# Performance work log

Hardware: AMD Instinct MI355X
Metric: run time of the kernel (lower is better)

Reference implementation:

```python
import jax, jax.numpy as jnp
import numpy as np

BATCH = 2
L = 2048
D_MODEL = 1024
D_STATE = 16
D_CONV = 4
EXPAND = 2
D_INNER = EXPAND * D_MODEL  # 2048
DT_RANK = (D_MODEL + 15) // 16  # 64


def setup_inputs() -> dict:
    key = jax.random.key(0)
    ks = jax.random.split(key, 12)
    f = jnp.float32
    hidden_states = jax.random.normal(ks[0], (BATCH, L, D_MODEL), f)
    input2 = jax.random.normal(ks[1], (BATCH, L, D_MODEL), f)
    in_proj1_w = jax.random.normal(ks[2], (D_INNER, D_MODEL), f) * (D_MODEL ** -0.5)
    in_proj2_w = jax.random.normal(ks[3], (D_INNER, D_MODEL), f) * (D_MODEL ** -0.5)
    conv_w = jax.random.normal(ks[4], (D_INNER, 1, D_CONV), f) * (D_CONV ** -0.5)
    conv_b = jax.random.normal(ks[5], (D_INNER,), f) * 0.02
    x_proj_w = jax.random.normal(ks[6], (DT_RANK + 2 * D_STATE, D_INNER), f) * (D_INNER ** -0.5)
    dt_std = DT_RANK ** -0.5
    dt_proj_w = jax.random.uniform(ks[7], (D_INNER, DT_RANK), f, -dt_std, dt_std)
    # dt bias init: inverse softplus of log-uniform dt in [1e-3, 1e-1]
    dt = jnp.exp(jax.random.uniform(ks[8], (D_INNER,), f) * (np.log(0.1) - np.log(0.001)) + np.log(0.001))
    dt = jnp.clip(dt, 1e-4, None)
    dt_proj_b = dt + jnp.log(-jnp.expm1(-dt))
    # A_log init: log(1..d_state) broadcast over channels
    A_log = jnp.log(jnp.broadcast_to(jnp.arange(1, D_STATE + 1, dtype=f), (D_INNER, D_STATE)))
    D = jnp.ones((D_INNER,), f)
    out_proj_w = jax.random.normal(ks[9], (D_MODEL, D_INNER), f) * (D_INNER ** -0.5)
    return dict(hidden_states=hidden_states, input2=input2, in_proj1_w=in_proj1_w,
                in_proj2_w=in_proj2_w, conv_w=conv_w, conv_b=conv_b, x_proj_w=x_proj_w,
                dt_proj_w=dt_proj_w, dt_proj_b=dt_proj_b, A_log=A_log, D=D,
                out_proj_w=out_proj_w)


def _forward(hidden_states, input2, in_proj1_w, in_proj2_w, conv_w, conv_b,
             x_proj_w, dt_proj_w, dt_proj_b, A_log, D, out_proj_w):
    # in_proj: (B,L,Dm) -> (B,d_inner,L)
    x = jnp.einsum('bld,ed->bel', hidden_states, in_proj1_w)
    z = jnp.einsum('bld,ed->bel', input2, in_proj2_w)
    # causal depthwise conv1d (left pad d_conv-1, equiv to torch pad+truncate) + SiLU
    xc = jax.lax.conv_general_dilated(x, conv_w, (1,), [(D_CONV - 1, 0)],
                                      dimension_numbers=('NCH', 'OIH', 'NCH'),
                                      feature_group_count=D_INNER)
    x = jax.nn.silu(xc + conv_b[None, :, None])
    # x_proj -> dt, B, C
    x_dbl = jnp.einsum('bel,re->brl', x, x_proj_w)  # (B, dt_rank+2n, L)
    dt = x_dbl[:, :DT_RANK]
    Bm = x_dbl[:, DT_RANK:DT_RANK + D_STATE]       # (B, n, L)
    Cm = x_dbl[:, DT_RANK + D_STATE:]               # (B, n, L)
    delta = jnp.einsum('brl,er->bel', dt, dt_proj_w)
    delta = jax.nn.softplus(delta + dt_proj_b[None, :, None])  # (B, d_inner, L)
    A = -jnp.exp(A_log)  # (d_inner, n)
    # selective scan over time (time-major for lax.scan)
    dlt = jnp.transpose(delta, (2, 0, 1))  # (L, B, d)
    u = jnp.transpose(x, (2, 0, 1))        # (L, B, d)
    Bt = jnp.transpose(Bm, (2, 0, 1))      # (L, B, n)
    Ct = jnp.transpose(Cm, (2, 0, 1))      # (L, B, n)

    def step(state, inp):
        d_t, u_t, B_t, C_t = inp
        dA = jnp.exp(d_t[..., None] * A)                        # (B, d, n)
        state = state * dA + (d_t * u_t)[..., None] * B_t[:, None, :]
        y_t = jnp.einsum('bdn,bn->bd', state, C_t)
        return state, y_t

    init = jnp.zeros((hidden_states.shape[0], D_INNER, D_STATE), x.dtype)
    _, ys = jax.lax.scan(step, init, (dlt, u, Bt, Ct))
    y = jnp.transpose(ys, (1, 2, 0)) + D[None, :, None] * x  # (B, d, L)
    y = y * jax.nn.silu(z)
    out = jnp.einsum('bel,de->bld', y, out_proj_w)  # out_proj, no bias
    return out


def reference(hidden_states, input2, in_proj1_w, in_proj2_w, conv_w, conv_b,
              x_proj_w, dt_proj_w, dt_proj_b, A_log, D, out_proj_w):
    return _forward(hidden_states, input2, in_proj1_w, in_proj2_w, conv_w, conv_b,
                    x_proj_w, dt_proj_w, dt_proj_b, A_log, D, out_proj_w)
```

## Files before the change

### kernel.cpp

```cpp
#include <hip/hip_runtime.h>
#include <cstddef>
#include <cmath>
#include <type_traits>

#define BATCH 2
#define LSEQ 2048
#define DM 1024
#define DSTATE 16
#define DI 2048
#define DTR 64
#define XDR 96
#define NC 64
#define TC 32
#define PN (4096 * 96)

using f32x4 = __attribute__((ext_vector_type(4))) float;
using bf16x8 = __attribute__((ext_vector_type(8))) short;

__device__ __forceinline__ unsigned short f2bf(float f) {
  union { float f; unsigned int u; } c; c.f = f;
  unsigned int u = c.u;
  return (unsigned short)((u + 0x7FFFu + ((u >> 16) & 1u)) >> 16);
}
__device__ __forceinline__ float bf2f(unsigned short h) {
  union { unsigned int u; float f; } c; c.u = ((unsigned int)h) << 16;
  return c.f;
}
__device__ __forceinline__ unsigned int pack2(float a, float b) {
  return (unsigned int)f2bf(a) | ((unsigned int)f2bf(b) << 16);
}

__device__ __forceinline__ void gl_lds16(const void* g, void* l) {
  __builtin_amdgcn_global_load_lds(
      (const __attribute__((address_space(1))) void*)g,
      (__attribute__((address_space(3))) void*)l, 16, 0, 0);
}

__device__ __forceinline__ float softplus_fast(float x) {
  float ex = __expf(x);
  return (x > 20.f) ? x : __logf(1.f + ex);
}

__device__ __forceinline__ void pow_tree(float q1, float* dA) {
  float q2 = q1 * q1;
  float q3 = q2 * q1;
  float q4 = q2 * q2;
  float q8 = q4 * q4;
  float q5 = q4 * q1, q6 = q4 * q2, q7 = q4 * q3;
  dA[0] = q1;  dA[1] = q2;  dA[2] = q3;  dA[3] = q4;
  dA[4] = q5;  dA[5] = q6;  dA[6] = q7;  dA[7] = q8;
  dA[8] = q8 * q1;  dA[9] = q8 * q2;  dA[10] = q8 * q3;  dA[11] = q8 * q4;
  dA[12] = q8 * q5; dA[13] = q8 * q6; dA[14] = q8 * q7;  dA[15] = q8 * q8;
}

__global__ __launch_bounds__(256) void cvt_bf16_kernel(
    const float* __restrict__ s, unsigned short* __restrict__ d, int n8) {
  int i = blockIdx.x * 256 + threadIdx.x;
  if (i >= n8) return;
  const float4* sp = reinterpret_cast<const float4*>(s) + (size_t)i * 2;
  float4 a = sp[0], b = sp[1];
  uint4 v = make_uint4(pack2(a.x, a.y), pack2(a.z, a.w), pack2(b.x, b.y),
                       pack2(b.z, b.w));
  *(reinterpret_cast<uint4*>(d) + i) = v;
}

template <typename OutT>
__global__ __launch_bounds__(256) void gemm_bf16_t(
    const unsigned short* __restrict__ A, const unsigned short* __restrict__ B,
    OutT* __restrict__ C, int K, int lda, int ldb, int ldc) {
  __shared__ __align__(16) unsigned short As[128][64];
  __shared__ __align__(16) unsigned short Bs[128][64];

  const int tid = threadIdx.x;
  const int lane = tid & 63;
  const int w = tid >> 6;

  const int gx = gridDim.x;
  const int nwg = gx * gridDim.y;
  const int id = blockIdx.y * gx + blockIdx.x;
  const int cpx = nwg >> 3;
  const int lt = (id & 7) * cpx + (id >> 3);
  const size_t m0 = (size_t)(lt / gx) * 128;
  const size_t n0 = (size_t)(lt % gx) * 128;

  const int rsub = lane >> 3;
  const int sslot = (lane & 7) ^ rsub;
  const unsigned short* Ab = A + m0 * lda + (size_t)rsub * lda + sslot * 8;
  const unsigned short* Bb = B + n0 * ldb + (size_t)rsub * ldb + sslot * 8;

  f32x4 acc[4][4] = {};

  const int fr = lane & 15;
  const int q = lane >> 4;
  const int f7 = fr & 7;

  for (int k0 = 0; k0 < K; k0 += 64) {
#pragma unroll
    for (int i = 0; i < 4; ++i) {
      const int r0 = w * 32 + i * 8;
      gl_lds16(Ab + (size_t)r0 * lda + k0, &As[r0][0]);
      gl_lds16(Bb + (size_t)r0 * ldb + k0, &Bs[r0][0]);
    }
    __syncthreads();

    bf16x8 af[4][2], bf_[4][2];
#pragma unroll
    for (int i = 0; i < 4; ++i) {
#pragma unroll
      for (int kk = 0; kk < 2; ++kk) {
        const int sA = (((kk * 4 + q) ^ f7) << 3);
        af[i][kk] = *reinterpret_cast<const bf16x8*>(
            &As[(w >> 1) * 64 + i * 16 + fr][sA]);
        bf_[i][kk] = *reinterpret_cast<const bf16x8*>(
            &Bs[(w & 1) * 64 + i * 16 + fr][sA]);
      }
    }
#pragma unroll
    for (int kk = 0; kk < 2; ++kk)
#pragma unroll
      for (int i = 0; i < 4; ++i)
#pragma unroll
        for (int j = 0; j < 4; ++j)
          acc[i][j] = __builtin_amdgcn_mfma_f32_16x16x32_bf16(
              af[i][kk], bf_[j][kk], acc[i][j], 0, 0, 0);
    __syncthreads();
  }

  const int crb = q * 4;
#pragma unroll
  for (int i = 0; i < 4; ++i) {
    size_t row = m0 + (w >> 1) * 64 + i * 16 + crb;
#pragma unroll
    for (int j = 0; j < 4; ++j) {
      size_t col = n0 + (w & 1) * 64 + j * 16 + fr;
#pragma unroll
      for (int r = 0; r < 4; ++r) {
        if constexpr (std::is_same_v<OutT, unsigned short>)
          C[(row + r) * ldc + col] = f2bf(acc[i][j][r]);
        else
          C[(row + r) * ldc + col] = acc[i][j][r];
      }
    }
  }
}

__global__ __launch_bounds__(256) void gemm_delta(
    const unsigned short* __restrict__ A, const unsigned short* __restrict__ B,
    const float* __restrict__ bias, unsigned short* __restrict__ C, int K,
    int lda, int ldb, int ldc) {
  __shared__ __align__(16) unsigned short As[128][64];
  __shared__ __align__(16) unsigned short Bs[128][64];

  const int tid = threadIdx.x;
  const int lane = tid & 63;
  const int w = tid >> 6;

  const int gx = gridDim.x;
  const int nwg = gx * gridDim.y;
  const int id = blockIdx.y * gx + blockIdx.x;
  const int cpx = nwg >> 3;
  const int lt = (id & 7) * cpx + (id >> 3);
  const size_t m0 = (size_t)(lt / gx) * 128;
  const size_t n0 = (size_t)(lt % gx) * 128;

  const int rsub = lane >> 3;
  const int sslot = (lane & 7) ^ rsub;
  const unsigned short* Ab = A + m0 * lda + (size_t)rsub * lda + sslot * 8;
  const unsigned short* Bb = B + n0 * ldb + (size_t)rsub * ldb + sslot * 8;

  f32x4 acc[4][4] = {};

  const int fr = lane & 15;
  const int q = lane >> 4;
  const int f7 = fr & 7;

  for (int k0 = 0; k0 < K; k0 += 64) {
#pragma unroll
    for (int i = 0; i < 4; ++i) {
      const int r0 = w * 32 + i * 8;
      gl_lds16(Ab + (size_t)r0 * lda + k0, &As[r0][0]);
      gl_lds16(Bb + (size_t)r0 * ldb + k0, &Bs[r0][0]);
    }
    __syncthreads();

    bf16x8 af[4][2], bf_[4][2];
#pragma unroll
    for (int i = 0; i < 4; ++i) {
#pragma unroll
      for (int kk = 0; kk < 2; ++kk) {
        const int sA = (((kk * 4 + q) ^ f7) << 3);
        af[i][kk] = *reinterpret_cast<const bf16x8*>(
            &As[(w >> 1) * 64 + i * 16 + fr][sA]);
        bf_[i][kk] = *reinterpret_cast<const bf16x8*>(
            &Bs[(w & 1) * 64 + i * 16 + fr][sA]);
      }
    }
#pragma unroll
    for (int kk = 0; kk < 2; ++kk)
#pragma unroll
      for (int i = 0; i < 4; ++i)
#pragma unroll
        for (int j = 0; j < 4; ++j)
          acc[i][j] = __builtin_amdgcn_mfma_f32_16x16x32_bf16(
              af[i][kk], bf_[j][kk], acc[i][j], 0, 0, 0);
    __syncthreads();
  }

  const int crb = q * 4;
#pragma unroll
  for (int i = 0; i < 4; ++i) {
    size_t row = m0 + (w >> 1) * 64 + i * 16 + crb;
#pragma unroll
    for (int j = 0; j < 4; ++j) {
      size_t col = n0 + (w & 1) * 64 + j * 16 + fr;
      float bv = bias[col];
#pragma unroll
      for (int r = 0; r < 4; ++r)
        C[(row + r) * ldc + col] = f2bf(softplus_fast(acc[i][j][r] + bv));
    }
  }
}

__global__ __launch_bounds__(256) void gemm_xdbl(
    const unsigned short* __restrict__ A,
    const unsigned short* __restrict__ B,
    float* __restrict__ P) {
  __shared__ __align__(16) unsigned short As[128][64];
  __shared__ __align__(16) unsigned short Bs[96][64];

  const int tid = threadIdx.x;
  const int lane = tid & 63;
  const int w = tid >> 6;
  const size_t m0 = (size_t)blockIdx.x * 128;
  const int k0base = blockIdx.y * 512;

  const int rsub = lane >> 3;
  const int sslot = (lane & 7) ^ rsub;
  const unsigned short* Ab = A + m0 * DI + (size_t)rsub * DI + sslot * 8;
  const unsigned short* Bb = B + (size_t)rsub * DI + sslot * 8;

  f32x4 acc[4][3] = {};

  const int fr = lane & 15;
  const int q = lane >> 4;
  const int f7 = fr & 7;

  for (int ks = 0; ks < 8; ++ks) {
    const int k0 = k0base + ks * 64;
#pragma unroll
    for (int i = 0; i < 4; ++i) {
      const int r0 = w * 32 + i * 8;
      gl_lds16(Ab + (size_t)r0 * DI + k0, &As[r0][0]);
    }
#pragma unroll
    for (int i = 0; i < 3; ++i) {
      const int r0 = w * 24 + i * 8;
      gl_lds16(Bb + (size_t)r0 * DI + k0, &Bs[r0][0]);
    }
    __syncthreads();

    bf16x8 af[4][2], bf_[3][2];
#pragma unroll
    for (int kk = 0; kk < 2; ++kk) {
      const int sA = (((kk * 4 + q) ^ f7) << 3);
#pragma unroll
      for (int i = 0; i < 4; ++i)
        af[i][kk] = *reinterpret_cast<const bf16x8*>(
            &As[(w >> 1) * 64 + i * 16 + fr][sA]);
#pragma unroll
      for (int j = 0; j < 3; ++j)
        bf_[j][kk] = *reinterpret_cast<const bf16x8*>(
            &Bs[(w & 1) * 48 + j * 16 + fr][sA]);
    }
#pragma unroll
    for (int kk = 0; kk < 2; ++kk)
#pragma unroll
      for (int i = 0; i < 4; ++i)
#pragma unroll
        for (int j = 0; j < 3; ++j)
          acc[i][j] = __builtin_amdgcn_mfma_f32_16x16x32_bf16(
              af[i][kk], bf_[j][kk], acc[i][j], 0, 0, 0);
    __syncthreads();
  }

  float* Pz = P + (size_t)blockIdx.y * PN;
  const int crb = q * 4;
#pragma unroll
  for (int i = 0; i < 4; ++i) {
    size_t row = m0 + (w >> 1) * 64 + i * 16 + crb;
#pragma unroll
    for (int j = 0; j < 3; ++j) {
      int col = (w & 1) * 48 + j * 16 + fr;
#pragma unroll
      for (int r = 0; r < 4; ++r) Pz[(row + r) * XDR + col] = acc[i][j][r];
    }
  }
}

__global__ __launch_bounds__(256) void reduce4x_kernel(
    const float* __restrict__ P, unsigned short* __restrict__ dtB,
    float* __restrict__ BC) {
  int i = blockIdx.x * 256 + threadIdx.x;
  int row = i / XDR, col = i - row * XDR;
  float s = (P[i] + P[PN + i]) + (P[2 * PN + i] + P[3 * PN + i]);
  if (col < 64)
    dtB[row * 64 + col] = f2bf(s);
  else
    BC[row * 32 + (col - 64)] = s;
}

__global__ __launch_bounds__(256) void conv_silu_kernel(
    const float* __restrict__ x, const float* __restrict__ w,
    const float* __restrict__ cb, unsigned short* __restrict__ out) {
  int idx = blockIdx.x * 256 + threadIdx.x;
  int e4 = idx % (DI / 4);
  int bl = idx / (DI / 4);
  int l = bl % LSEQ;
  int e = e4 * 4;

  const float4* cw = reinterpret_cast<const float4*>(w);
  float4 w0 = cw[e], w1 = cw[e + 1], w2 = cw[e + 2], w3 = cw[e + 3];
  float4 acc = *reinterpret_cast<const float4*>(&cb[e]);

#define TAPK(K, COMP)                                                       \
  {                                                                         \
    int ls = l - 3 + (K);                                                   \
    if (ls >= 0) {                                                          \
      float4 xv = *reinterpret_cast<const float4*>(                         \
          &x[((size_t)(bl) - 3 + (K)) * DI + e]);                           \
      acc.x = fmaf(xv.x, w0.COMP, acc.x);                                   \
      acc.y = fmaf(xv.y, w1.COMP, acc.y);                                   \
      acc.z = fmaf(xv.z, w2.COMP, acc.z);                                   \
      acc.w = fmaf(xv.w, w3.COMP, acc.w);                                   \
    }                                                                       \
  }
  TAPK(0, x)
  TAPK(1, y)
  TAPK(2, z)
  TAPK(3, w)
#undef TAPK

  acc.x = acc.x / (1.f + expf(-acc.x));
  acc.y = acc.y / (1.f + expf(-acc.y));
  acc.z = acc.z / (1.f + expf(-acc.z));
  acc.w = acc.w / (1.f + expf(-acc.w));
  *reinterpret_cast<uint2*>(&out[(size_t)bl * DI + e]) =
      make_uint2(pack2(acc.x, acc.y), pack2(acc.z, acc.w));
}

__global__ __launch_bounds__(256) void scan_passA(
    const unsigned short* __restrict__ dB, const unsigned short* __restrict__ u,
    const float* __restrict__ bc, const float* __restrict__ A_log,
    float* __restrict__ sEnd, float* __restrict__ sProd) {
  int g = blockIdx.x * 256 + threadIdx.x;
  int e = g & (DI - 1);
  int c = (g >> 11) & (NC - 1);
  int b = g >> 17;

  const float nA0 = -__expf(A_log[e * DSTATE]);
  bool aok = true;
#pragma unroll
  for (int n = 1; n < DSTATE; ++n) {
    float nAn = -__expf(A_log[e * DSTATE + n]);
    aok = aok && (fabsf(nAn - (float)(n + 1) * nA0) <= 1e-4f * fabsf(nAn));
  }

  size_t off = ((size_t)b * LSEQ + c * TC) * DI + e;
  size_t boff = ((size_t)b * LSEQ + c * TC) * 32;

  float s[DSTATE], P[DSTATE];
#pragma unroll
  for (int n = 0; n < DSTATE; ++n) { s[n] = 0.f; P[n] = 1.f; }

  float d = bf2f(dB[off]);
  float ut = bf2f(u[off]);

  for (int t = 0; t < TC; ++t) {
    float d_n = 0.f, ut_n = 0.f;
    if (t + 1 < TC) {
      d_n = bf2f(dB[off + DI]);
      ut_n = bf2f(u[off + DI]);
    }

    float db = d * ut;
    float dA[DSTATE];
    if (aok) {
      pow_tree(__expf(d * nA0), dA);
    } else {
#pragma unroll
      for (int n = 0; n < DSTATE; ++n)
        dA[n] = __expf(-d * __expf(A_log[e * DSTATE + n]));
    }
    const float4* bcp = reinterpret_cast<const float4*>(&bc[boff]);
    float4 B0 = bcp[0], B1 = bcp[1], B2 = bcp[2], B3 = bcp[3];
    float Bv[DSTATE] = {B0.x, B0.y, B0.z, B0.w, B1.x, B1.y, B1.z, B1.w,
                        B2.x, B2.y, B2.z, B2.w, B3.x, B3.y, B3.z, B3.w};
#pragma unroll
    for (int n = 0; n < DSTATE; ++n) {
      s[n] = fmaf(s[n], dA[n], db * Bv[n]);
      P[n] *= dA[n];
    }
    off += DI;
    boff += 32;
    d = d_n; ut = ut_n;
  }

  size_t o = (((size_t)b * NC + c) * DI + e) * DSTATE;
  float4* se = reinterpret_cast<float4*>(&sEnd[o]);
  float4* sp = reinterpret_cast<float4*>(&sProd[o]);
  se[0] = make_float4(s[0], s[1], s[2], s[3]);
  se[1] = make_float4(s[4], s[5], s[6], s[7]);
  se[2] = make_float4(s[8], s[9], s[10], s[11]);
  se[3] = make_float4(s[12], s[13], s[14], s[15]);
  sp[0] = make_float4(P[0], P[1], P[2], P[3]);
  sp[1] = make_float4(P[4], P[5], P[6], P[7]);
  sp[2] = make_float4(P[8], P[9], P[10], P[11]);
  sp[3] = make_float4(P[12], P[13], P[14], P[15]);
}

__global__ __launch_bounds__(256) void scan_passB(
    float* __restrict__ sEnd, const float* __restrict__ sProd) {
  int g = blockIdx.x * 256 + threadIdx.x;
  int n = g & 15;
  int e = (g >> 4) & (DI - 1);
  int b = g >> 15;
  float s = 0.f;
  for (int c = 0; c < NC; ++c) {
    size_t o = (((size_t)b * NC + c) * DI + e) * DSTATE + n;
    float se = sEnd[o];
    float sp = sProd[o];
    sEnd[o] = s;
    s = fmaf(s, sp, se);
  }
}

__global__ __launch_bounds__(256) void scan_passC(
    const unsigned short* __restrict__ dB, const unsigned short* __restrict__ u,
    const unsigned short* __restrict__ z, const float* __restrict__ bc,
    const float* __restrict__ A_log, const float* __restrict__ Dv,
    const float* __restrict__ sInit, unsigned short* __restrict__ gOut) {
  int g = blockIdx.x * 256 + threadIdx.x;
  int e = g & (DI - 1);
  int c = (g >> 11) & (NC - 1);
  int b = g >> 17;

  const float nA0 = -__expf(A_log[e * DSTATE]);
  bool aok = true;
#pragma unroll
  for (int n = 1; n < DSTATE; ++n) {
    float nAn = -__expf(A_log[e * DSTATE + n]);
    aok = aok && (fabsf(nAn - (float)(n + 1) * nA0) <= 1e-4f * fabsf(nAn));
  }
  const float Dval = Dv[e];

  size_t off = ((size_t)b * LSEQ + c * TC) * DI + e;
  size_t boff = ((size_t)b * LSEQ + c * TC) * 32;

  float s[DSTATE];
  {
    size_t o = (((size_t)b * NC + c) * DI + e) * DSTATE;
    const float4* si = reinterpret_cast<const float4*>(&sInit[o]);
    float4 s0 = si[0], s1 = si[1], s2 = si[2], s3 = si[3];
    s[0] = s0.x; s[1] = s0.y; s[2] = s0.z; s[3] = s0.w;
    s[4] = s1.x; s[5] = s1.y; s[6] = s1.z; s[7] = s1.w;
    s[8] = s2.x; s[9] = s2.y; s[10] = s2.z; s[11] = s2.w;
    s[12] = s3.x; s[13] = s3.y; s[14] = s3.z; s[15] = s3.w;
  }

  float d = bf2f(dB[off]);
  float ut = bf2f(u[off]);
  float zt = bf2f(z[off]);

  for (int t = 0; t < TC; ++t) {
    float d_n = 0.f, ut_n = 0.f, zt_n = 0.f;
    if (t + 1 < TC) {
      d_n = bf2f(dB[off + DI]);
      ut_n = bf2f(u[off + DI]);
      zt_n = bf2f(z[off + DI]);
    }

    float db = d * ut;
    float dA[DSTATE];
    if (aok) {
      pow_tree(__expf(d * nA0), dA);
    } else {
#pragma unroll
      for (int n = 0; n < DSTATE; ++n)
        dA[n] = __expf(-d * __expf(A_log[e * DSTATE + n]));
    }
    const float4* bcp = reinterpret_cast<const float4*>(&bc[boff]);
    float4 B0 = bcp[0], B1 = bcp[1], B2 = bcp[2], B3 = bcp[3];
    float4 C0 = bcp[4], C1 = bcp[5], C2 = bcp[6], C3 = bcp[7];
    float Bv[DSTATE] = {B0.x, B0.y, B0.z, B0.w, B1.x, B1.y, B1.z, B1.w,
                        B2.x, B2.y, B2.z, B2.w, B3.x, B3.y, B3.z, B3.w};
    float Cv[DSTATE] = {C0.x, C0.y, C0.z, C0.w, C1.x, C1.y, C1.z, C1.w,
                        C2.x, C2.y, C2.z, C2.w, C3.x, C3.y, C3.z, C3.w};
    float y0 = 0.f, y1 = 0.f, y2 = 0.f, y3 = 0.f;
#pragma unroll
    for (int n = 0; n < 4; ++n) {
      s[n] = fmaf(s[n], dA[n], db * Bv[n]);
      y0 = fmaf(s[n], Cv[n], y0);
      s[n + 4] = fmaf(s[n + 4], dA[n + 4], db * Bv[n + 4]);
      y1 = fmaf(s[n + 4], Cv[n + 4], y1);
      s[n + 8] = fmaf(s[n + 8], dA[n + 8], db * Bv[n + 8]);
      y2 = fmaf(s[n + 8], Cv[n + 8], y2);
      s[n + 12] = fmaf(s[n + 12], dA[n + 12], db * Bv[n + 12]);
      y3 = fmaf(s[n + 12], Cv[n + 12], y3);
    }
    float y = (y0 + y1) + (y2 + y3);
    float gate = zt / (1.f + __expf(-zt));
    gOut[off] = f2bf((y + Dval * ut) * gate);

    off += DI;
    boff += 32;
    d = d_n; ut = ut_n; zt = zt_n;
  }
}

extern "C" void kernel_launch(void* const* d_in, const int* in_sizes, int n_in,
                              void* d_out, int out_size, void* d_ws,
                              size_t ws_size, hipStream_t stream) {
  const float* hs = (const float*)d_in[0];
  const float* in2 = (const float*)d_in[1];
  const float* w1 = (const float*)d_in[2];
  const float* w2 = (const float*)d_in[3];
  const float* cw = (const float*)d_in[4];
  const float* cb = (const float*)d_in[5];
  const float* xpw = (const float*)d_in[6];
  const float* dtw = (const float*)d_in[7];
  const float* dtb = (const float*)d_in[8];
  const float* alog = (const float*)d_in[9];
  const float* Dv = (const float*)d_in[10];
  const float* ow = (const float*)d_in[11];
  float* out = (float*)d_out;

  const size_t BLE = (size_t)BATCH * LSEQ * DI;
  const size_t BLM = (size_t)BATCH * LSEQ * DM;
  const size_t WN = (size_t)DI * DM;
  const size_t SC = (size_t)BATCH * NC * DI * DSTATE;

  float* W = (float*)d_ws;
  float* bufX = W;
  float* M2 = W + BLE;
  float* M3 = M2 + BLE / 2;
  float* M4 = M3 + BLE / 2;
  float* sEnd = M4 + BLE / 2;
  float* sProd = sEnd + SC;
  float* BC = sProd + SC;

  unsigned short* hsb = (unsigned short*)M2;
  unsigned short* zb = (unsigned short*)M2;
  unsigned short* in2b = (unsigned short*)M3;
  unsigned short* ub = (unsigned short*)M3;
  unsigned short* wb1 = (unsigned short*)M4;
  unsigned short* wb2 = wb1 + WN;
  float* xdblP = M4;
  unsigned short* xpwB = (unsigned short*)(M4 + 4 * PN);
  unsigned short* dtB = (unsigned short*)(M4 + 4 * PN + 98304 + 16);
  unsigned short* dtwB = (unsigned short*)(M4 + 4 * PN + 98304 + 131072 + 32);
  unsigned short* bufG = (unsigned short*)M4;
  unsigned short* dB = (unsigned short*)bufX;
  unsigned short* owb = (unsigned short*)sProd;

  const int M = BATCH * LSEQ;
  dim3 blk(256);

  cvt_bf16_kernel<<<(int)(BLM / 8 / 256), blk, 0, stream>>>(hs, hsb,
                                                            (int)(BLM / 8));
  cvt_bf16_kernel<<<(int)(BLM / 8 / 256), blk, 0, stream>>>(in2, in2b,
                                                            (int)(BLM / 8));
  cvt_bf16_kernel<<<(int)(WN / 8 / 256), blk, 0, stream>>>(w1, wb1,
                                                           (int)(WN / 8));
  cvt_bf16_kernel<<<(int)(WN / 8 / 256), blk, 0, stream>>>(w2, wb2,
                                                           (int)(WN / 8));
  gemm_bf16_t<float><<<dim3(DI / 128, M / 128), blk, 0, stream>>>(
      hsb, wb1, bufX, DM, DM, DM, DI);
  gemm_bf16_t<unsigned short><<<dim3(DI / 128, M / 128), blk, 0, stream>>>(
      in2b, wb2, zb, DM, DM, DM, DI);
  conv_silu_kernel<<<(M * (DI / 4)) / 256, blk, 0, stream>>>(bufX, cw, cb, ub);
  cvt_bf16_kernel<<<96, blk, 0, stream>>>(xpw, xpwB, XDR * DI / 8);
  cvt_bf16_kernel<<<64, blk, 0, stream>>>(dtw, dtwB, DI * DTR / 8);
  gemm_xdbl<<<dim3(M / 128, 4), blk, 0, stream>>>(ub, xpwB, xdblP);
  reduce4x_kernel<<<(M * XDR) / 256, blk, 0, stream>>>(xdblP, dtB, BC);
  gemm_delta<<<dim3(DI / 128, M / 128), blk, 0, stream>>>(
      dtB, dtwB, dtb, dB, DTR, DTR, DTR, DI);
  scan_passA<<<(BATCH * DI * NC) / 256, blk, 0, stream>>>(dB, ub, BC, alog,
                                                          sEnd, sProd);
  scan_passB<<<(BATCH * DI * DSTATE) / 256, blk, 0, stream>>>(sEnd, sProd);
  cvt_bf16_kernel<<<(int)(WN / 8 / 256), blk, 0, stream>>>(ow, owb,
                                                           (int)(WN / 8));
  scan_passC<<<(BATCH * DI * NC) / 256, blk, 0, stream>>>(
      dB, ub, zb, BC, alog, Dv, sEnd, bufG);
  gemm_bf16_t<float><<<dim3(DM / 128, M / 128), blk, 0, stream>>>(
      bufG, owb, out, DI, DI, DI, DM);
}
```

Measured before the change: 247.0 us.

## Split scan state dimension across thread pairs with shuffle reduction

Scan passes A and C now assign each (batch, channel, chunk) to two adjacent threads, each owning 8 of the 16 state elements, doubling the thread count. Pass C combines the partial output dot products with a lane shuffle, and only the even lane writes the gated result. The aim is more parallelism and lower per-thread register pressure in the sequential scan. In exchange, dB, u and z loads and the exp/pow work are duplicated across the pair, and adjacent lanes now touch the same channel, which changes coalescing of the bf16 loads and stores.

```diff
diff --git a/kernel.cpp b/kernel.cpp
--- a/kernel.cpp
+++ b/kernel.cpp
@@ -39,18 +39,6 @@
 __device__ __forceinline__ float softplus_fast(float x) {
   float ex = __expf(x);
   return (x > 20.f) ? x : __logf(1.f + ex);
-}
-
-__device__ __forceinline__ void pow_tree(float q1, float* dA) {
-  float q2 = q1 * q1;
-  float q3 = q2 * q1;
-  float q4 = q2 * q2;
-  float q8 = q4 * q4;
-  float q5 = q4 * q1, q6 = q4 * q2, q7 = q4 * q3;
-  dA[0] = q1;  dA[1] = q2;  dA[2] = q3;  dA[3] = q4;
-  dA[4] = q5;  dA[5] = q6;  dA[6] = q7;  dA[7] = q8;
-  dA[8] = q8 * q1;  dA[9] = q8 * q2;  dA[10] = q8 * q3;  dA[11] = q8 * q4;
-  dA[12] = q8 * q5; dA[13] = q8 * q6; dA[14] = q8 * q7;  dA[15] = q8 * q8;
 }
 
 __global__ __launch_bounds__(256) void cvt_bf16_kernel(
@@ -353,9 +341,10 @@
     const float* __restrict__ bc, const float* __restrict__ A_log,
     float* __restrict__ sEnd, float* __restrict__ sProd) {
   int g = blockIdx.x * 256 + threadIdx.x;
-  int e = g & (DI - 1);
-  int c = (g >> 11) & (NC - 1);
-  int b = g >> 17;
+  int h = g & 1;
+  int e = (g >> 1) & (DI - 1);
+  int c = (g >> 12) & (NC - 1);
+  int b = g >> 18;
 
   const float nA0 = -__expf(A_log[e * DSTATE]);
   bool aok = true;
@@ -366,11 +355,11 @@
   }
 
   size_t off = ((size_t)b * LSEQ + c * TC) * DI + e;
-  size_t boff = ((size_t)b * LSEQ + c * TC) * 32;
-
-  float s[DSTATE], P[DSTATE];
-#pragma unroll
-  for (int n = 0; n < DSTATE; ++n) { s[n] = 0.f; P[n] = 1.f; }
+  size_t boff = ((size_t)b * LSEQ + c * TC) * 32 + h * 8;
+
+  float s[8], P[8];
+#pragma unroll
+  for (int j = 0; j < 8; ++j) { s[j] = 0.f; P[j] = 1.f; }
 
   float d = bf2f(dB[off]);
   float ut = bf2f(u[off]);
@@ -383,39 +372,40 @@
     }
 
     float db = d * ut;
-    float dA[DSTATE];
+    float dA[8];
     if (aok) {
-      pow_tree(__expf(d * nA0), dA);
+      float q1 = __expf(d * nA0);
+      float q2 = q1 * q1, q3 = q2 * q1, q4 = q2 * q2;
+      float q5 = q4 * q1, q6 = q4 * q2, q7 = q4 * q3, q8 = q4 * q4;
+      float base = h ? q8 : 1.0f;
+      dA[0] = q1 * base; dA[1] = q2 * base; dA[2] = q3 * base;
+      dA[3] = q4 * base; dA[4] = q5 * base; dA[5] = q6 * base;
+      dA[6] = q7 * base; dA[7] = q8 * base;
     } else {
 #pragma unroll
-      for (int n = 0; n < DSTATE; ++n)
-        dA[n] = __expf(-d * __expf(A_log[e * DSTATE + n]));
+      for (int j = 0; j < 8; ++j)
+        dA[j] = __expf(-d * __expf(A_log[e * DSTATE + h * 8 + j]));
     }
     const float4* bcp = reinterpret_cast<const float4*>(&bc[boff]);
-    float4 B0 = bcp[0], B1 = bcp[1], B2 = bcp[2], B3 = bcp[3];
-    float Bv[DSTATE] = {B0.x, B0.y, B0.z, B0.w, B1.x, B1.y, B1.z, B1.w,
-                        B2.x, B2.y, B2.z, B2.w, B3.x, B3.y, B3.z, B3.w};
-#pragma unroll
-    for (int n = 0; n < DSTATE; ++n) {
-      s[n] = fmaf(s[n], dA[n], db * Bv[n]);
-      P[n] *= dA[n];
+    float4 B0 = bcp[0], B1 = bcp[1];
+    float Bv[8] = {B0.x, B0.y, B0.z, B0.w, B1.x, B1.y, B1.z, B1.w};
+#pragma unroll
+    for (int j = 0; j < 8; ++j) {
+      s[j] = fmaf(s[j], dA[j], db * Bv[j]);
+      P[j] *= dA[j];
     }
     off += DI;
     boff += 32;
     d = d_n; ut = ut_n;
   }
 
-  size_t o = (((size_t)b * NC + c) * DI + e) * DSTATE;
+  size_t o = (((size_t)b * NC + c) * DI + e) * DSTATE + h * 8;
   float4* se = reinterpret_cast<float4*>(&sEnd[o]);
   float4* sp = reinterpret_cast<float4*>(&sProd[o]);
   se[0] = make_float4(s[0], s[1], s[2], s[3]);
   se[1] = make_float4(s[4], s[5], s[6], s[7]);
-  se[2] = make_float4(s[8], s[9], s[10], s[11]);
-  se[3] = make_float4(s[12], s[13], s[14], s[15]);
   sp[0] = make_float4(P[0], P[1], P[2], P[3]);
   sp[1] = make_float4(P[4], P[5], P[6], P[7]);
-  sp[2] = make_float4(P[8], P[9], P[10], P[11]);
-  sp[3] = make_float4(P[12], P[13], P[14], P[15]);
 }
 
 __global__ __launch_bounds__(256) void scan_passB(
@@ -440,9 +430,10 @@
     const float* __restrict__ A_log, const float* __restrict__ Dv,
     const float* __restrict__ sInit, unsigned short* __restrict__ gOut) {
   int g = blockIdx.x * 256 + threadIdx.x;
-  int e = g & (DI - 1);
-  int c = (g >> 11) & (NC - 1);
-  int b = g >> 17;
+  int h = g & 1;
+  int e = (g >> 1) & (DI - 1);
+  int c = (g >> 12) & (NC - 1);
+  int b = g >> 18;
 
   const float nA0 = -__expf(A_log[e * DSTATE]);
   bool aok = true;
@@ -454,17 +445,15 @@
   const float Dval = Dv[e];
 
   size_t off = ((size_t)b * LSEQ + c * TC) * DI + e;
-  size_t boff = ((size_t)b * LSEQ + c * TC) * 32;
-
-  float s[DSTATE];
+  size_t boff = ((size_t)b * LSEQ + c * TC) * 32 + h * 8;
+
+  float s[8];
   {
-    size_t o = (((size_t)b * NC + c) * DI + e) * DSTATE;
+    size_t o = (((size_t)b * NC + c) * DI + e) * DSTATE + h * 8;
     const float4* si = reinterpret_cast<const float4*>(&sInit[o]);
-    float4 s0 = si[0], s1 = si[1], s2 = si[2], s3 = si[3];
+    float4 s0 = si[0], s1 = si[1];
     s[0] = s0.x; s[1] = s0.y; s[2] = s0.z; s[3] = s0.w;
     s[4] = s1.x; s[5] = s1.y; s[6] = s1.z; s[7] = s1.w;
-    s[8] = s2.x; s[9] = s2.y; s[10] = s2.z; s[11] = s2.w;
-    s[12] = s3.x; s[13] = s3.y; s[14] = s3.z; s[15] = s3.w;
   }
 
   float d = bf2f(dB[off]);
@@ -480,36 +469,39 @@
     }
 
     float db = d * ut;
-    float dA[DSTATE];
+    float dA[8];
     if (aok) {
-      pow_tree(__expf(d * nA0), dA);
+      float q1 = __expf(d * nA0);
+      float q2 = q1 * q1, q3 = q2 * q1, q4 = q2 * q2;
+      float q5 = q4 * q1, q6 = q4 * q2, q7 = q4 * q3, q8 = q4 * q4;
+      float base = h ? q8 : 1.0f;
+      dA[0] = q1 * base; dA[1] = q2 * base; dA[2] = q3 * base;
+      dA[3] = q4 * base; dA[4] = q5 * base; dA[5] = q6 * base;
+      dA[6] = q7 * base; dA[7] = q8 * base;
     } else {
 #pragma unroll
-      for (int n = 0; n < DSTATE; ++n)
-        dA[n] = __expf(-d * __expf(A_log[e * DSTATE + n]));
+      for (int j = 0; j < 8; ++j)
+        dA[j] = __expf(-d * __expf(A_log[e * DSTATE + h * 8 + j]));
     }
     const float4* bcp = reinterpret_cast<const float4*>(&bc[boff]);
-    float4 B0 = bcp[0], B1 = bcp[1], B2 = bcp[2], B3 = bcp[3];
-    float4 C0 = bcp[4], C1 = bcp[5], C2 = bcp[6], C3 = bcp[7];
-    float Bv[DSTATE] = {B0.x, B0.y, B0.z, B0.w, B1.x, B1.y, B1.z, B1.w,
-                        B2.x, B2.y, B2.z, B2.w, B3.x, B3.y, B3.z, B3.w};
-    float Cv[DSTATE] = {C0.x, C0.y, C0.z, C0.w, C1.x, C1.y, C1.z, C1.w,
-                        C2.x, C2.y, C2.z, C2.w, C3.x, C3.y, C3.z, C3.w};
-    float y0 = 0.f, y1 = 0.f, y2 = 0.f, y3 = 0.f;
-#pragma unroll
-    for (int n = 0; n < 4; ++n) {
-      s[n] = fmaf(s[n], dA[n], db * Bv[n]);
-      y0 = fmaf(s[n], Cv[n], y0);
-      s[n + 4] = fmaf(s[n + 4], dA[n + 4], db * Bv[n + 4]);
-      y1 = fmaf(s[n + 4], Cv[n + 4], y1);
-      s[n + 8] = fmaf(s[n + 8], dA[n + 8], db * Bv[n + 8]);
-      y2 = fmaf(s[n + 8], Cv[n + 8], y2);
-      s[n + 12] = fmaf(s[n + 12], dA[n + 12], db * Bv[n + 12]);
-      y3 = fmaf(s[n + 12], Cv[n + 12], y3);
-    }
-    float y = (y0 + y1) + (y2 + y3);
-    float gate = zt / (1.f + __expf(-zt));
-    gOut[off] = f2bf((y + Dval * ut) * gate);
+    float4 B0 = bcp[0], B1 = bcp[1];
+    float4 C0 = bcp[4], C1 = bcp[5];
+    float Bv[8] = {B0.x, B0.y, B0.z, B0.w, B1.x, B1.y, B1.z, B1.w};
+    float Cv[8] = {C0.x, C0.y, C0.z, C0.w, C1.x, C1.y, C1.z, C1.w};
+    float yA = 0.f, yB = 0.f;
+#pragma unroll
+    for (int j = 0; j < 4; ++j) {
+      s[j] = fmaf(s[j], dA[j], db * Bv[j]);
+      yA = fmaf(s[j], Cv[j], yA);
+      s[j + 4] = fmaf(s[j + 4], dA[j + 4], db * Bv[j + 4]);
+      yB = fmaf(s[j + 4], Cv[j + 4], yB);
+    }
+    float yh = yA + yB;
+    float y = yh + __shfl_xor(yh, 1);
+    if (h == 0) {
+      float gate = zt / (1.f + __expf(-zt));
+      gOut[off] = f2bf((y + Dval * ut) * gate);
+    }
 
     off += DI;
     boff += 32;
@@ -584,12 +576,12 @@
   reduce4x_kernel<<<(M * XDR) / 256, blk, 0, stream>>>(xdblP, dtB, BC);
   gemm_delta<<<dim3(DI / 128, M / 128), blk, 0, stream>>>(
       dtB, dtwB, dtb, dB, DTR, DTR, DTR, DI);
-  scan_passA<<<(BATCH * DI * NC) / 256, blk, 0, stream>>>(dB, ub, BC, alog,
-                                                          sEnd, sProd);
+  scan_passA<<<(BATCH * DI * NC * 2) / 256, blk, 0, stream>>>(dB, ub, BC, alog,
+                                                              sEnd, sProd);
   scan_passB<<<(BATCH * DI * DSTATE) / 256, blk, 0, stream>>>(sEnd, sProd);
   cvt_bf16_kernel<<<(int)(WN / 8 / 256), blk, 0, stream>>>(ow, owb,
                                                            (int)(WN / 8));
-  scan_passC<<<(BATCH * DI * NC) / 256, blk, 0, stream>>>(
+  scan_passC<<<(BATCH * DI * NC * 2) / 256, blk, 0, stream>>>(
       dB, ub, zb, BC, alog, Dv, sEnd, bufG);
   gemm_bf16_t<float><<<dim3(DM / 128, M / 128), blk, 0, stream>>>(
       bufG, owb, out, DI, DI, DI, DM);
```

Measured after the change: 250.8 us. About the same (+1.5%).
